# Kernel tuning notes

Measured on AMD Instinct MI355X. Metric: run time of the kernel, lower is better.

## Reference

```python
import jax, jax.numpy as jnp
import numpy as np

DIM = 128        # channel width
HEAD_DIM = 8     # LiteMLA dim per head
BN_EPS = 1e-5
ATT_EPS = 1e-15


def conv2d(x, w, b=None, groups=1):
    # x: NCHW, w: OIHW; stride 1, SAME padding (matches pad=k//2 in torch)
    y = jax.lax.conv_general_dilated(
        x, w, (1, 1), "SAME",
        dimension_numbers=("NCHW", "OIHW", "NCHW"),
        feature_group_count=groups)
    return y if b is None else y + b[None, :, None, None]


def bn_eval(x, g, b, m, v):
    scale = g * jax.lax.rsqrt(v + BN_EPS)
    return (x - m[None, :, None, None]) * scale[None, :, None, None] + b[None, :, None, None]


def hswish(x):
    return x * jnp.clip(x + 3.0, 0.0, 6.0) * (1.0 / 6.0)


def relu_linear_att(qkv):
    # qkv: [B, G*3*d, H, W] with d = HEAD_DIM
    B, C, H, W = qkv.shape
    d = HEAD_DIM
    qkv = qkv.reshape(B, -1, 3 * d, H * W)          # [B, G, 3d, N]
    q = jax.nn.relu(qkv[:, :, :d])                  # [B, G, d, N]
    k = jax.nn.relu(qkv[:, :, d:2 * d])             # [B, G, d, N]
    v = qkv[:, :, 2 * d:]                           # [B, G, d, N]
    v = jnp.concatenate([v, jnp.ones_like(v[:, :, :1])], axis=2)  # pad ones row -> [B, G, d+1, N]
    kv = jnp.einsum("bgdn,bgen->bgde", v, k)        # [B, G, d+1, d]
    out = jnp.einsum("bgde,bgen->bgdn", kv, q)      # [B, G, d+1, N]
    out = out[:, :, :d] / (out[:, :, d:d + 1] + ATT_EPS)
    return out.reshape(B, -1, H, W)                 # [B, G*d, H, W]


def setup_inputs() -> dict:
    key = jax.random.key(0)
    ks = jax.random.split(key, 24)
    dim = DIM
    mid = 6 * dim
    B, H, W = 4, 128, 128

    def w(k, shape, s=0.05):
        return jax.random.normal(k, shape, jnp.float32) * s

    return {
        "ref_features": jax.random.normal(ks[0], (B, dim, H, W), jnp.float32),
        "other_features": jax.random.normal(ks[1], (B, dim, H, W), jnp.float32),
        # 3x3 QKV projection convs (dim -> total_dim = dim)
        "wq": w(ks[2], (dim, dim, 3, 3)), "bq": w(ks[3], (dim,)),
        "wk": w(ks[4], (dim, dim, 3, 3)), "bk": w(ks[5], (dim,)),
        "wv": w(ks[6], (dim, dim, 3, 3)), "bv": w(ks[7], (dim,)),
        # multi-scale aggreg (scale=5): depthwise 5x5 + grouped 1x1 (groups = 3*heads)
        "agg_dw_w": w(ks[8], (3 * dim, 1, 5, 5)),
        "agg_pw_w": w(ks[9], (3 * dim, HEAD_DIM, 1, 1)),
        # attention output proj: 1x1 (2*dim -> dim), no bias, + BN
        "attn_proj_w": w(ks[10], (dim, 2 * dim, 1, 1)),
        "bn1_g": 1.0 + w(ks[11], (dim,)), "bn1_b": w(ks[12], (dim,)),
        "bn1_m": w(ks[13], (dim,), 0.1),
        "bn1_v": jax.random.uniform(ks[14], (dim,), jnp.float32, 0.5, 1.5),
        # MBConv: expand 1x1 (bias, hswish), depthwise 3x3 (bias, hswish), project 1x1 (no bias) + BN
        "mb1_w": w(ks[15], (mid, dim, 1, 1)), "mb1_b": w(ks[16], (mid,)),
        "mb2_w": w(ks[17], (mid, 1, 3, 3)), "mb2_b": w(ks[18], (mid,)),
        "mb3_w": w(ks[19], (dim, mid, 1, 1)),
        "bn2_g": 1.0 + w(ks[20], (dim,)), "bn2_b": w(ks[21], (dim,)),
        "bn2_m": w(ks[22], (dim,), 0.1),
        "bn2_v": jax.random.uniform(ks[23], (dim,), jnp.float32, 0.5, 1.5),
    }


def reference(ref_features, other_features, wq, bq, wk, bk, wv, bv,
              agg_dw_w, agg_pw_w, attn_proj_w, bn1_g, bn1_b, bn1_m, bn1_v,
              mb1_w, mb1_b, mb2_w, mb2_b, mb3_w, bn2_g, bn2_b, bn2_m, bn2_v):
    dim = DIM
    heads = dim // HEAD_DIM
    # QKV via 3x3 convs and concat
    q = conv2d(ref_features, wq, bq)
    k = conv2d(other_features, wk, bk)
    v = conv2d(other_features, wv, bv)
    qkv = jnp.concatenate([q, k, v], axis=1)               # [B, 3*dim, H, W]
    # multi-scale branch (scale 5)
    ms = conv2d(qkv, agg_dw_w, groups=3 * dim)             # depthwise 5x5
    ms = conv2d(ms, agg_pw_w, groups=3 * heads)            # grouped 1x1
    multi = jnp.concatenate([qkv, ms], axis=1)             # [B, 6*dim, H, W]
    # ReLU linear attention + proj(1x1) + BN
    att = relu_linear_att(multi)                           # [B, 2*dim, H, W]
    att = bn_eval(conv2d(att, attn_proj_w), bn1_g, bn1_b, bn1_m, bn1_v)
    attended = ref_features + att
    # local module: residual MBConv
    h = hswish(conv2d(attended, mb1_w, mb1_b))
    h = hswish(conv2d(h, mb2_w, mb2_b, groups=6 * dim))
    h = bn_eval(conv2d(h, mb3_w), bn2_g, bn2_b, bn2_m, bn2_v)
    return attended + h
```

## Files before the change

### kernel.cpp

```cpp
#include <hip/hip_runtime.h>
#include <hip/hip_bf16.h>

#define HH 128
#define WW 128
#define NPIX 16384

using bf16 = __hip_bfloat16;
typedef __attribute__((ext_vector_type(8))) short short8;
typedef __attribute__((ext_vector_type(4))) float f32x4;

__device__ __forceinline__ float b2f(bf16 x){ return __bfloat162float(x); }
__device__ __forceinline__ bf16 f2b(float x){ return __float2bfloat16(x); }
__device__ __forceinline__ unsigned short f2bu(float x){
  bf16 h = __float2bfloat16(x);
  return __builtin_bit_cast(unsigned short, h);
}
__device__ __forceinline__ unsigned short bbits(bf16 x){
  return __builtin_bit_cast(unsigned short, x);
}
__device__ __forceinline__ float u16f(unsigned short u){
  return __bfloat162float(__builtin_bit_cast(bf16, u));
}
__device__ __forceinline__ unsigned int relu2(unsigned int x){
  unsigned int s = x & 0x80008000u;
  unsigned int t = s >> 15;
  unsigned int m = (t << 16) - t;
  return x & ~m;
}
__device__ __forceinline__ float hswish(float x){
  float t = fminf(fmaxf(x + 3.0f, 0.0f), 6.0f);
  return x * t * (1.0f/6.0f);
}

__global__ __launch_bounds__(256) void k_wprep(
    const float* __restrict__ wq, const float* __restrict__ wk,
    const float* __restrict__ wv, const float* __restrict__ bq,
    const float* __restrict__ bk, const float* __restrict__ bv,
    const float* __restrict__ w1, const float* __restrict__ w3,
    bf16* __restrict__ wbf2, float* __restrict__ biasc,
    bf16* __restrict__ w1b, bf16* __restrict__ w3b)
{
  const int idx = blockIdx.x*256 + (int)threadIdx.x;
  if (idx < 384)
    biasc[idx] = (idx < 128) ? bq[idx] : (idx < 256 ? bk[idx-128] : bv[idx-256]);
  if (idx < 98304) {
    w1b[idx] = f2b(w1[idx]);
    w3b[idx] = f2b(w3[idx]);
  }
  if (idx < 384*1152) {
    const int c = idx / 1152, rem = idx % 1152;
    const int tap = rem >> 7, ci = rem & 127;
    const float* wsrc = (c < 128) ? wq : (c < 256 ? wk : wv);
    const int cl = (c < 128) ? c : (c < 256 ? c-128 : c-256);
    wbf2[idx] = f2b(wsrc[(size_t)cl*1152 + ci*9 + tap]);
  }
}

__global__ __launch_bounds__(256) void k_nhwc(
    const float* __restrict__ refB, const float* __restrict__ othB,
    bf16* __restrict__ nh)
{
  const int pt = blockIdx.x & 127;
  const int sidx = blockIdx.x >> 7;
  const float* src = sidx ? othB : refB;
  __shared__ unsigned short t[128][130];
  const int tid = threadIdx.x;
  const int px4 = (tid & 31) * 4;
  const int cq = tid >> 5;
  #pragma unroll
  for (int cb = 0; cb < 16; ++cb) {
    const int c = cb*8 + cq;
    const float4 f = *(const float4*)(src + (size_t)c*NPIX + pt*128 + px4);
    t[px4+0][c] = f2bu(f.x); t[px4+1][c] = f2bu(f.y);
    t[px4+2][c] = f2bu(f.z); t[px4+3][c] = f2bu(f.w);
// ... 62 lines not shown

  #pragma unroll
  for (int cb = 0; cb < 4; ++cb) {
    __syncthreads();
    #pragma unroll
    for (int row = 0; row < 3; ++row) {
      *(uint4*)&lds[row*RSTR + ldsw]     = cur[row][0];
      *(uint4*)&lds[row*RSTR + ldsw + 8] = cur[row][1];
    }
    __syncthreads();
    if (cb < 3) {
      #pragma unroll
      for (int row = 0; row < 3; ++row) {
        const int yy = y + row - 1;
        if (yy >= 0 && yy < HH) {
          const bf16* p = src + (size_t)(yy*WW + sx)*128 + (cb+1)*32 + sp*16;
          nxt[row][0] = *(const uint4*)(p);
          nxt[row][1] = *(const uint4*)(p + 8);
        } else { nxt[row][0] = z4; nxt[row][1] = z4; }
      }
    }
    #pragma unroll
    for (int tap = 0; tap < 9; ++tap) {
      const int trow = tap/3, kx = tap%3;
      const short8 af = *(const short8*)(wbf2
          + (size_t)(cw + l15)*1152 + tap*128 + cb*32 + qd*8);
      const int bbase = trow*RSTR + (l15 + kx)*CSTR + qd*8;
      #pragma unroll
      for (int g = 0; g < 8; ++g) {
        const short8 bfr = *(const short8*)&lds[bbase + g*16*CSTR];
        acc[g] = __builtin_amdgcn_mfma_f32_16x16x32_bf16(af, bfr, acc[g], 0, 0, 0);
      }
    }
    #pragma unroll
    for (int row = 0; row < 3; ++row) {
      cur[row][0] = nxt[row][0];
      cur[row][1] = nxt[row][1];
    }
  }
  #pragma unroll
  for (int r = 0; r < 4; ++r) {
    const int c = cw + qd*4 + r;
    const int gg = c / 24, rr = c % 24;
    bf16* outp = (rr < 8) ? (qbuf + (size_t)(gg*8 + rr)*NPIX)
                          : (kvbuf + (size_t)(gg*16 + (rr-8))*NPIX);
    const float bias = biasc[c];
    #pragma unroll
    for (int g = 0; g < 8; ++g)
      outp[y*WW + g*16 + l15] = f2b(acc[g][r] + bias);
  }
}

#define KVSTR 520
#define ATT_SMEM_BYTES 37120
__global__ __launch_bounds__(256) void k_att_ms(
    const bf16* __restrict__ kvbuf, const bf16* __restrict__ qbuf,
    const float* __restrict__ adw, const float* __restrict__ apw,
    float* __restrict__ part, bf16* __restrict__ msq)
{
  __shared__ __align__(16) unsigned char smem[ATT_SMEM_BYTES];
  const int br = blockIdx.x % 3;
  const int sub = blockIdx.x / 3;
  const int tid = threadIdx.x;
  const int lane = tid & 63;
  const int w = tid >> 6;
  const int qd = lane >> 4, l15 = lane & 15;

  if (br == 0) {
    const int s = sub & 31;
    const int gl = sub >> 5;
    const bf16* bp = kvbuf + (size_t)gl*16*NPIX;
    float (*redm)[9][8] = (float(*)[9][8])smem;
    const int k0 = s*512 + w*128 + qd*8;
    const bf16* ap = bp + (size_t)(8 + (l15 & 7))*NPIX + k0;
    const bf16* bk = bp + (size_t)(l15 & 7)*NPIX + k0;
    const short8 ones8 = {0x3F80,0x3F80,0x3F80,0x3F80,0x3F80,0x3F80,0x3F80,0x3F80};
    f32x4 mac = (f32x4){0.f,0.f,0.f,0.f};
    #pragma unroll
    for (int m = 0; m < 4; ++m) {
      short8 av = *(const short8*)(ap + m*32);
      if (l15 == 8) av = ones8;
      uint4 bu = *(const uint4*)(bk + m*32);
      bu.x = relu2(bu.x); bu.y = relu2(bu.y);
      bu.z = relu2(bu.z); bu.w = relu2(bu.w);
      const short8 bv = __builtin_bit_cast(short8, bu);
      mac = __builtin_amdgcn_mfma_f32_16x16x32_bf16(av, bv, mac, 0, 0, 0);
    }
    #pragma unroll
    for (int r = 0; r < 4; ++r) {
      const int row = qd*4 + r;
      if (l15 < 8 && row < 9) redm[w][row][l15] = mac[r];
    }
    __syncthreads();
    if (tid < 72)
      part[((size_t)gl*32 + s)*72 + tid] =
          redm[0][tid>>3][tid&7] + redm[1][tid>>3][tid&7]
        + redm[2][tid>>3][tid&7] + redm[3][tid>>3][tid&7];

  } else if (br == 1) {
    const int t  = sub & 31;
    const int jj = sub >> 5;
    unsigned short (*sIn)[1056] = (unsigned short(*)[1056])smem;
    float (*dww)[25] = (float(*)[25])(smem + 33792);
    float (*pww)[8]  = (float(*)[8])(smem + 35392);
    float (*redm)[9][8] = (float(*)[9][8])(smem + 35904);
    unsigned short* kvA = (unsigned short*)smem;
    unsigned short* kvB = kvA + 16*KVSTR;

    for (int i = tid; i < 400; i += 256) {
      const int ch = i/25, kk5 = i%25;
      dww[ch][kk5] = adw[(24*jj + 8 + ch)*25 + kk5];
    }
    for (int i = tid; i < 128; i += 256) {
      const int r = i>>3, ii = i&7;
      pww[r][ii] = apw[(24*jj + 8 + r)*8 + ii];
    }
    if (tid < 128) {
      const int ch = tid & 15, r = tid >> 4;
      sIn[ch][r*132 + 0] = 0; sIn[ch][r*132 + 1] = 0;
      sIn[ch][r*132 + 130] = 0; sIn[ch][r*132 + 131] = 0;
    }
    const int y0 = t*4 - 2;
    #pragma unroll
    for (int rep = 0; rep < 8; ++rep) {
      const int L = rep*256 + tid;
      const int col8 = L & 15;
      const int rowc = L >> 4;
      const int r = rowc >> 4, ch = rowc & 15;
      const int gy = y0 + r;
      uint4 pk = make_uint4(0u,0u,0u,0u);
      if (gy >= 0 && gy < HH)
        pk = *(const uint4*)(kvbuf + (size_t)(jj*16 + ch)*NPIX + gy*WW + col8*8);
      unsigned short* dst = &sIn[ch][r*132 + 2 + col8*8];
      *(unsigned int*)(dst + 0) = pk.x;
      *(unsigned int*)(dst + 2) = pk.y;
      *(unsigned int*)(dst + 4) = pk.z;
      *(unsigned int*)(dst + 6) = pk.w;
    }
    __syncthreads();

    const int x = tid & 127;
    const int h = tid >> 7;
    const int rbase = h*2;

    float ko[8][2];
    #pragma unroll
    for (int e=0;e<8;++e){ ko[e][0]=0.f; ko[e][1]=0.f; }
    #pragma unroll
    for (int c=0;c<8;++c) {
      float o0=0.f, o1=0.f;
      #pragma unroll
      for (int rr=0; rr<6; ++rr) {
        const unsigned short* rp = &sIn[c][(rbase+rr)*132 + x];
        #pragma unroll
        for (int dx=0; dx<5; ++dx) {
          const float v = u16f(rp[dx]);
          if (rr <= 4) o0 += dww[c][rr*5+dx]*v;
          if (rr >= 1) o1 += dww[c][(rr-1)*5+dx]*v;
        }
      }
      #pragma unroll
      for (int e=0;e<8;++e){ ko[e][0] += pww[e][c]*o0; ko[e][1] += pww[e][c]*o1; }
    }
    #pragma unroll
    for (int e=0;e<8;++e){ ko[e][0]=fmaxf(ko[e][0],0.f); ko[e][1]=fmaxf(ko[e][1],0.f); }

    float dv[8][2];
    #pragma unroll
    for (int c=0;c<8;++c) {
      float o0=0.f, o1=0.f;
      #pragma unroll
      for (int rr=0; rr<6; ++rr) {
        const unsigned short* rp = &sIn[8+c][(rbase+rr)*132 + x];
        #pragma unroll
        for (int dx=0; dx<5; ++dx) {
          const float v = u16f(rp[dx]);
          if (rr <= 4) o0 += dww[8+c][rr*5+dx]*v;
          if (rr >= 1) o1 += dww[8+c][(rr-1)*5+dx]*v;
        }
      }
      dv[c][0]=o0; dv[c][1]=o1;
    }
    float mv[8][2];
    #pragma unroll
    for (int d=0;d<8;++d) {
      float v0=0.f, v1=0.f;
      #pragma unroll
      for (int i=0;i<8;++i){ v0 += pww[8+d][i]*dv[i][0]; v1 += pww[8+d][i]*dv[i][1]; }
      mv[d][0]=v0; mv[d][1]=v1;
    }

    __syncthreads();
    #pragma unroll
    for (int rr=0; rr<2; ++rr) {
      const int px = (h*2+rr)*128 + x;
      #pragma unroll
      for (int e=0;e<8;++e) kvB[e*KVSTR + px] = f2bu(ko[e][rr]);
      #pragma unroll
      for (int d=0;d<8;++d) kvA[d*KVSTR + px] = f2bu(mv[d][rr]);
      kvA[8*KVSTR + px] = 0x3F80;
    }
    __syncthreads();

    f32x4 mac = (f32x4){0.f,0.f,0.f,0.f};
    #pragma unroll
    for (int m = 0; m < 4; ++m) {
      const int kk = w*128 + m*32 + qd*8;
      const short8 av = *(const short8*)&kvA[l15*KVSTR + kk];
      const short8 bv = *(const short8*)&kvB[l15*KVSTR + kk];
      mac = __builtin_amdgcn_mfma_f32_16x16x32_bf16(av, bv, mac, 0, 0, 0);
    }
    #pragma unroll
    for (int r = 0; r < 4; ++r) {
      const int row = qd*4 + r;
      if (l15 < 8 && row < 9) redm[w][row][l15] = mac[r];
    }
    __syncthreads();
    if (tid < 72)
      part[((size_t)(16+jj)*32 + t)*72 + tid] =
          redm[0][tid>>3][tid&7] + redm[1][tid>>3][tid&7]
        + redm[2][tid>>3][tid&7] + redm[3][tid>>3][tid&7];

  } else {
    const int t  = sub & 31;
    const int jj = sub >> 5;
    unsigned short (*sIn)[1056] = (unsigned short(*)[1056])smem;
    float (*dww)[25] = (float(*)[25])(smem + 16896);
    float (*pww)[8]  = (float(*)[8])(smem + 17696);

    for (int i = tid; i < 200; i += 256)
      dww[i/25][i%25] = adw[(24*jj + i/25)*25 + (i%25)];
    if (tid < 64)
      pww[tid>>3][tid&7] = apw[(24*jj + (tid>>3))*8 + (tid&7)];
    if (tid < 64) {
      const int ch = tid & 7, r = tid >> 3;
      sIn[ch][r*132 + 0] = 0; sIn[ch][r*132 + 1] = 0;
      sIn[ch][r*132 + 130] = 0; sIn[ch][r*132 + 131] = 0;
    }
    const int y0 = t*4 - 2;
    #pragma unroll
    for (int rep = 0; rep < 4; ++rep) {
      const int L = rep*256 + tid;
      const int col8 = L & 15;
      const int rowc = L >> 4;
      const int r = rowc >> 3, ch = rowc & 7;
      const int gy = y0 + r;
      uint4 pk = make_uint4(0u,0u,0u,0u);
      if (gy >= 0 && gy < HH)
        pk = *(const uint4*)(qbuf + (size_t)(jj*8 + ch)*NPIX + gy*WW + col8*8);
      unsigned short* dst = &sIn[ch][r*132 + 2 + col8*8];
      *(unsigned int*)(dst + 0) = pk.x;
      *(unsigned int*)(dst + 2) = pk.y;
      *(unsigned int*)(dst + 4) = pk.z;
      *(unsigned int*)(dst + 6) = pk.w;
    }
    __syncthreads();

    const int x = tid & 127;
    const int h = tid >> 7;
    const int rbase = h*2;
    const int row0 = t*4 + h*2;

    float dq[8][2];
    #pragma unroll
    for (int c=0;c<8;++c) {
      float o0=0.f, o1=0.f;
      #pragma unroll
      for (int rr=0; rr<6; ++rr) {
        const unsigned short* rp = &sIn[c][(rbase+rr)*132 + x];
        #pragma unroll
        for (int dx=0; dx<5; ++dx) {
          const float v = u16f(rp[dx]);
          if (rr <= 4) o0 += dww[c][rr*5+dx]*v;
          if (rr >= 1) o1 += dww[c][(rr-1)*5+dx]*v;
        }
      }
      dq[c][0]=o0; dq[c][1]=o1;
    }
    #pragma unroll
    for (int e=0;e<8;++e) {
      float o0=0.f, o1=0.f;
      #pragma unroll
      for (int i=0;i<8;++i){ o0 += pww[e][i]*dq[i][0]; o1 += pww[e][i]*dq[i][1]; }
      bf16* op = msq + (size_t)(jj*8 + e)*NPIX + row0*WW + x;
      op[0]  = f2b(o0);
      op[WW] = f2b(o1);
    }
  }
}

__global__ __launch_bounds__(256) void k_fold2(
    const float* __restrict__ pjw, const float* __restrict__ part,
    const float* __restrict__ g1, const float* __restrict__ bb1,
    const float* __restrict__ m1, const float* __restrict__ v1,
    bf16* __restrict__ wtb, float* __restrict__ bias2, float* __restrict__ kvf)
{
  const int co = blockIdx.x;
  const int ge = (int)threadIdx.x;
  const int g = ge >> 3, e = ge & 7;
  float kv[8];
  #pragma unroll
  for (int d=0;d<8;++d) kv[d] = 0.f;
  for (int s = 0; s < 32; ++s) {
    const float* pp = part + ((size_t)g*32 + s)*72;
    #pragma unroll
    for (int d=0;d<8;++d) kv[d] += pp[d*8 + e];
  }
  const float sc = g1[co] * rsqrtf(v1[co] + 1e-5f);
  float acc = 0.f;
  #pragma unroll
  for (int d = 0; d < 8; ++d)
    acc += pjw[co*256 + g*8 + d] * kv[d];
  wtb[(size_t)co*256 + ge] = f2b(sc * acc);
  if (ge == 0) bias2[co] = bb1[co] - m1[co]*sc;
  if (co < 32 && ge < 8) {
    float s8 = 0.f;
    for (int s = 0; s < 32; ++s) s8 += part[((size_t)co*32 + s)*72 + 64 + ge];
    kvf[(size_t)co*72 + 64 + ge] = s8;
  }
}

__global__ __launch_bounds__(256) void k_proj_m(
    const bf16* __restrict__ qbuf, const bf16* __restrict__ msq,
    const float* __restrict__ kvf, const bf16* __restrict__ wtb,
    const float* __restrict__ bias2, const float* __restrict__ refB,
    float* __restrict__ attd)
{
  const int n0 = blockIdx.x * 64;
  __shared__ unsigned short lds[64*CSTR];
  __shared__ float kvden[32][8];
  __shared__ float b2s[128];
  const int tid = threadIdx.x;
  kvden[tid>>3][tid&7] = kvf[(size_t)(tid>>3)*72 + 64 + (tid&7)];
  if (tid < 128) b2s[tid] = bias2[tid];
  const int lane = tid & 63;
  const int w = tid >> 6;
  const int qd = lane >> 4, l15 = lane & 15;
  const int px = tid & 63;

// ... 41 lines not shown
      for (int gg = 0; gg < 4; ++gg) {
        const int pxg = n0 + gg*16 + l15;
        attd[(size_t)co*NPIX + pxg] = refB[(size_t)co*NPIX + pxg] + acc[t][gg][r] + bi;
      }
    }
  }
}

__global__ __launch_bounds__(256) void k_mb1_m(
    const float* __restrict__ attd, const bf16* __restrict__ w1b,
    const float* __restrict__ bias, bf16* __restrict__ h1s, int s)
{
  const int pxt = blockIdx.x & 127;
  const int cot = blockIdx.x >> 7;
  const int n0 = pxt*128;
  __shared__ unsigned short lds[128*CSTR];
  const int tid = threadIdx.x;
  const int lane = tid & 63;
  const int wv4 = tid >> 6;
  const int co16 = s*192 + cot*64 + wv4*16;
  const int qd = lane >> 4, l15 = lane & 15;
  f32x4 acc[8];
  #pragma unroll
  for (int g=0; g<8; ++g) acc[g] = (f32x4){0.f,0.f,0.f,0.f};
  const int sx = tid & 127, sp = tid >> 7;
  for (int cb = 0; cb < 4; ++cb) {
    __syncthreads();
    const float* rp = attd + (size_t)(cb*32)*NPIX + n0 + sx;
    for (int cp = sp; cp < 16; cp += 2) {
      const float a0 = rp[(size_t)(2*cp)*NPIX];
      const float a1 = rp[(size_t)(2*cp+1)*NPIX];
      *(unsigned int*)&lds[sx*CSTR + 2*cp] =
          ((unsigned int)f2bu(a1) << 16) | f2bu(a0);
    }
    __syncthreads();
    const short8 af = *(const short8*)(w1b + (size_t)(co16 + l15)*128 + cb*32 + qd*8);
    #pragma unroll
    for (int g = 0; g < 8; ++g) {
      const short8 bfr = *(const short8*)&lds[(g*16 + l15)*CSTR + qd*8];
      acc[g] = __builtin_amdgcn_mfma_f32_16x16x32_bf16(af, bfr, acc[g], 0, 0, 0);
    }
  }
  #pragma unroll
  for (int r = 0; r < 4; ++r) {
    const int co = co16 + qd*4 + r;
    const float bi = bias[co];
    bf16* op = h1s + (size_t)(co - s*192)*NPIX + n0;
    #pragma unroll
    for (int g = 0; g < 8; ++g)
      op[g*16 + l15] = f2b(hswish(acc[g][r] + bi));
  }
}

__global__ __launch_bounds__(256) void k_mb2(
    const bf16* __restrict__ h1s, const float* __restrict__ w,
    const float* __restrict__ bias, bf16* __restrict__ h2s, int s)
{
  const int rt = blockIdx.x & 3;
  const int cl = blockIdx.x >> 2;
  const int cg = s*192 + cl;
  __shared__ unsigned short tile[34][132];
  __shared__ float wc9[9];
  __shared__ float bsh[1];
  const int tid = threadIdx.x;
  if (tid < 9) wc9[tid] = w[cg*9 + tid];
  if (tid == 9) bsh[0] = bias[cg];
  if (tid < 136) {
    const int r = tid >> 2;
    const int csel = tid & 3;
    const int c = (csel == 0) ? 0 : (csel == 1) ? 1 : (csel == 2) ? 130 : 131;
    tile[r][c] = 0;
  }
  const int y0 = rt*32;
  const bf16* in = h1s + (size_t)cl*NPIX;
  for (int i = tid; i < 544; i += 256) {
    const int rr = i >> 4, c8 = i & 15;
    const int gy = y0 - 1 + rr;
    uint4 pk = make_uint4(0u,0u,0u,0u);
    if (gy >= 0 && gy < HH) pk = *(const uint4*)(in + gy*WW + c8*8);
    unsigned short* dst = &tile[rr][2 + c8*8];
    *(unsigned int*)(dst+0)=pk.x; *(unsigned int*)(dst+2)=pk.y;
    *(unsigned int*)(dst+4)=pk.z; *(unsigned int*)(dst+6)=pk.w;
  }
  __syncthreads();
  const int x = tid & 127;
  const int rb = (tid >> 7) * 16;
  float a0,b0,c0,a1,b1,c1,a2,b2,c2;
  {
    const unsigned short* p = &tile[rb][x+1];
    a0=u16f(p[0]); b0=u16f(p[1]); c0=u16f(p[2]);
    p = &tile[rb+1][x+1];
    a1=u16f(p[0]); b1=u16f(p[1]); c1=u16f(p[2]);
  }
  bf16* op = h2s + (size_t)cl*NPIX + (y0+rb)*WW + x;
  #pragma unroll
  for (int j = 0; j < 16; ++j) {
    const unsigned short* p = &tile[rb+j+2][x+1];
    a2=u16f(p[0]); b2=u16f(p[1]); c2=u16f(p[2]);
    float acc = bsh[0] + wc9[0]*a0 + wc9[1]*b0 + wc9[2]*c0
                       + wc9[3]*a1 + wc9[4]*b1 + wc9[5]*c1
                       + wc9[6]*a2 + wc9[7]*b2 + wc9[8]*c2;
    op[j*WW] = f2b(hswish(acc));
    a0=a1; b0=b1; c0=c1; a1=a2; b1=b2; c1=c2;
  }
}

__global__ __launch_bounds__(256) void k_mb31(
    const bf16* __restrict__ h2s, const bf16* __restrict__ w3b,
    float* __restrict__ accb, int s3,
    const float* __restrict__ attd, const bf16* __restrict__ w1b,
    const float* __restrict__ bias1, bf16* __restrict__ h1s, int s1)
{
  __shared__ unsigned short lds[128*CSTR];
  const int tid = threadIdx.x;
  const int lane = tid & 63;
  const int wv4 = tid >> 6;
  const int qd = lane >> 4, l15 = lane & 15;
  const int sx = tid & 127, sp = tid >> 7;

  if (blockIdx.x < 256) {
    const int pxt = blockIdx.x & 127;
    const int cot = blockIdx.x >> 7;
    const int n0 = pxt*128;
    const int co16 = cot*64 + wv4*16;
    f32x4 acc[8];
    #pragma unroll
    for (int g=0; g<8; ++g) acc[g] = (f32x4){0.f,0.f,0.f,0.f};
    for (int cb = 0; cb < 6; ++cb) {
      __syncthreads();
      const bf16* rp = h2s + (size_t)(cb*32)*NPIX + n0 + sx;
      for (int cp = sp; cp < 16; cp += 2) {
        const unsigned short a0 = bbits(rp[(size_t)(2*cp)*NPIX]);
        const unsigned short a1 = bbits(rp[(size_t)(2*cp+1)*NPIX]);
        *(unsigned int*)&lds[sx*CSTR + 2*cp] = ((unsigned int)a1 << 16) | a0;
      }
      __syncthreads();
      const short8 af = *(const short8*)(w3b + (size_t)(co16 + l15)*768 + s3*192 + cb*32 + qd*8);
      #pragma unroll
      for (int g = 0; g < 8; ++g) {
        const short8 bfr = *(const short8*)&lds[(g*16 + l15)*CSTR + qd*8];
        acc[g] = __builtin_amdgcn_mfma_f32_16x16x32_bf16(af, bfr, acc[g], 0, 0, 0);
      }
    }
    #pragma unroll
    for (int r = 0; r < 4; ++r) {
      const int co = co16 + qd*4 + r;
      float* op = accb + (size_t)co*NPIX + n0;
      if (s3 == 0) {
        #pragma unroll
        for (int g = 0; g < 8; ++g) op[g*16 + l15] = acc[g][r];
      } else {
        #pragma unroll
        for (int g = 0; g < 8; ++g) op[g*16 + l15] += acc[g][r];
      }
    }
  } else {
    const int bid = blockIdx.x - 256;
    const int pxt = bid & 127;
    const int cot = bid >> 7;
    const int n0 = pxt*128;
    const int co16 = s1*192 + cot*64 + wv4*16;
    f32x4 acc[8];
    #pragma unroll
    for (int g=0; g<8; ++g) acc[g] = (f32x4){0.f,0.f,0.f,0.f};
    for (int cb = 0; cb < 4; ++cb) {
      __syncthreads();
      const float* rp = attd + (size_t)(cb*32)*NPIX + n0 + sx;
      for (int cp = sp; cp < 16; cp += 2) {
        const float a0 = rp[(size_t)(2*cp)*NPIX];
        const float a1 = rp[(size_t)(2*cp+1)*NPIX];
        *(unsigned int*)&lds[sx*CSTR + 2*cp] =
            ((unsigned int)f2bu(a1) << 16) | f2bu(a0);
      }
      __syncthreads();
      const short8 af = *(const short8*)(w1b + (size_t)(co16 + l15)*128 + cb*32 + qd*8);
      #pragma unroll
      for (int g = 0; g < 8; ++g) {
        const short8 bfr = *(const short8*)&lds[(g*16 + l15)*CSTR + qd*8];
        acc[g] = __builtin_amdgcn_mfma_f32_16x16x32_bf16(af, bfr, acc[g], 0, 0, 0);
      }
    }
    #pragma unroll
    for (int r = 0; r < 4; ++r) {
      const int co = co16 + qd*4 + r;
      const float bi = bias1[co];
      bf16* op = h1s + (size_t)(co - s1*192)*NPIX + n0;
      #pragma unroll
      for (int g = 0; g < 8; ++g)
        op[g*16 + l15] = f2b(hswish(acc[g][r] + bi));
    }
  }
}

__global__ __launch_bounds__(256) void k_mb3f(
    const bf16* __restrict__ h2s, const bf16* __restrict__ w3b,
    const float* __restrict__ accb,
    const float* __restrict__ g2, const float* __restrict__ b2p,
    const float* __restrict__ m2, const float* __restrict__ v2,
    float* __restrict__ attd)
{
  const int pxt = blockIdx.x & 127;
  const int cot = blockIdx.x >> 7;
  const int n0 = pxt*128;
  __shared__ unsigned short lds[128*CSTR];
  const int tid = threadIdx.x;
  const int lane = tid & 63;
  const int wv4 = tid >> 6;
  const int co16 = cot*64 + wv4*16;
  const int qd = lane >> 4, l15 = lane & 15;
  f32x4 acc[8];
  #pragma unroll
  for (int g=0; g<8; ++g) acc[g] = (f32x4){0.f,0.f,0.f,0.f};
  const int sx = tid & 127, sp = tid >> 7;
  for (int cb = 0; cb < 6; ++cb) {
    __syncthreads();
    const bf16* rp = h2s + (size_t)(cb*32)*NPIX + n0 + sx;
    for (int cp = sp; cp < 16; cp += 2) {
      const unsigned short a0 = bbits(rp[(size_t)(2*cp)*NPIX]);
      const unsigned short a1 = bbits(rp[(size_t)(2*cp+1)*NPIX]);
      *(unsigned int*)&lds[sx*CSTR + 2*cp] = ((unsigned int)a1 << 16) | a0;
    }
    __syncthreads();
    const short8 af = *(const short8*)(w3b + (size_t)(co16 + l15)*768 + 576 + cb*32 + qd*8);
    #pragma unroll
    for (int g = 0; g < 8; ++g) {
      const short8 bfr = *(const short8*)&lds[(g*16 + l15)*CSTR + qd*8];
      acc[g] = __builtin_amdgcn_mfma_f32_16x16x32_bf16(af, bfr, acc[g], 0, 0, 0);
    }
  }
  #pragma unroll
  for (int r = 0; r < 4; ++r) {
    const int co = co16 + qd*4 + r;
    const float scale = g2[co] * rsqrtf(v2[co] + 1e-5f);
    const float bb = b2p[co];
    const float mm = m2[co];
    #pragma unroll
    for (int g = 0; g < 8; ++g) {
      const size_t idx = (size_t)co*NPIX + n0 + g*16 + l15;
      const float val = accb[idx] + acc[g][r];
      const float y = (val - mm)*scale + bb;
      attd[idx] = attd[idx] + y;
    }
  }
}

extern "C" void kernel_launch(void* const* d_in, const int* in_sizes, int n_in,
                              void* d_out, int out_size, void* d_ws, size_t ws_size,
                              hipStream_t stream)
{
  const float* ref = (const float*)d_in[0];
  const float* oth = (const float*)d_in[1];
  const float* wq  = (const float*)d_in[2];
  const float* bq  = (const float*)d_in[3];
  const float* wk  = (const float*)d_in[4];
  const float* bk  = (const float*)d_in[5];
  const float* wv  = (const float*)d_in[6];
  const float* bv  = (const float*)d_in[7];
  const float* adw = (const float*)d_in[8];
  const float* apw = (const float*)d_in[9];
  const float* pjw = (const float*)d_in[10];
  const float* g1  = (const float*)d_in[11];
  const float* b1  = (const float*)d_in[12];
  const float* m1  = (const float*)d_in[13];
  const float* v1  = (const float*)d_in[14];
  const float* w1  = (const float*)d_in[15];
  const float* bb1 = (const float*)d_in[16];
  const float* w2  = (const float*)d_in[17];
  const float* bb2 = (const float*)d_in[18];
  const float* w3  = (const float*)d_in[19];
  const float* g2  = (const float*)d_in[20];
  const float* b2p = (const float*)d_in[21];
  const float* m2  = (const float*)d_in[22];
  const float* v2  = (const float*)d_in[23];

  char* ws = (char*)d_ws;
  bf16*  wbf2  = (bf16*)(ws + 0);
  float* biasc = (float*)(ws + 884736);
  bf16*  w1b   = (bf16*)(ws + 886272);
  bf16*  w3b   = (bf16*)(ws + 1082880);
  bf16*  kvbuf = (bf16*)(ws + 1279488);
  bf16*  qbuf  = (bf16*)(ws + 9668096);
  bf16*  nh    = (bf16*)(ws + 13862400);
  bf16*  msq   = (bf16*)(ws + 13862400);
  float* part  = (float*)(ws + 22251008);
  float* kvf   = (float*)(ws + 22545920);
  bf16*  wtb   = (bf16*)(ws + 22555136);
  float* bias2 = (float*)(ws + 22620672);
  float* accb  = (float*)(ws + 1279488);
  bf16*  h1s   = (bf16*)(ws + 9668096);
  bf16*  h2s   = (bf16*)(ws + 15959552);

  k_wprep<<<1728, 256, 0, stream>>>(wq, wk, wv, bq, bk, bv, w1, w3, wbf2, biasc, w1b, w3b);

  for (int b = 0; b < 4; ++b) {
    const float* refB = ref + (size_t)b*128*NPIX;
    const float* othB = oth + (size_t)b*128*NPIX;
    float* attd = (float*)d_out + (size_t)b*128*NPIX;

    k_nhwc   <<<256,  256, 0, stream>>>(refB, othB, nh);
    k_conv   <<<768,  256, 0, stream>>>(nh, wbf2, biasc, kvbuf, qbuf);
    k_att_ms <<<1536, 256, 0, stream>>>(kvbuf, qbuf, adw, apw, part, msq);
    k_fold2  <<<128,  256, 0, stream>>>(pjw, part, g1, b1, m1, v1, wtb, bias2, kvf);
    k_proj_m <<<256,  256, 0, stream>>>(qbuf, msq, kvf, wtb, bias2, refB, attd);

    k_mb1_m  <<<384,  256, 0, stream>>>(attd, w1b, bb1, h1s, 0);
    k_mb2    <<<768,  256, 0, stream>>>(h1s, w2, bb2, h2s, 0);
    for (int s = 0; s < 3; ++s) {
      k_mb31 <<<640,  256, 0, stream>>>(h2s, w3b, accb, s, attd, w1b, bb1, h1s, s+1);
      k_mb2  <<<768,  256, 0, stream>>>(h1s, w2, bb2, h2s, s+1);
    }
    k_mb3f   <<<256,  256, 0, stream>>>(h2s, w3b, accb, g2, b2p, m2, v2, attd);
  }
}
```

Before: 919.5 us.

## Fuse depthwise 3x3 MBConv stage into the pointwise projection GEMM kernels

The standalone depthwise 3x3 kernel (k_mb2) is removed. Its computation now runs inside the 1x1 projection kernels: each block loads three halo rows of 32 channels, computes depthwise plus hswish into LDS, then feeds the result to MFMA. The h1 buffer is ping-ponged between two workspace slots, which removes the h2 round trip through global memory and four launches per batch. In exchange, blocks are now organised per image row with heavier LDS use (about 36 KB), and each block recomputes the depthwise conv for its own output-channel tile, so that work is duplicated across the two cot tiles.

```diff
diff --git a/kernel.cpp b/kernel.cpp
--- a/kernel.cpp
+++ b/kernel.cpp
@@ -568,96 +568,112 @@
   }
 }
 
-__global__ __launch_bounds__(256) void k_mb2(
-    const bf16* __restrict__ h1s, const float* __restrict__ w,
-    const float* __restrict__ bias, bf16* __restrict__ h2s, int s)
-{
-  const int rt = blockIdx.x & 3;
-  const int cl = blockIdx.x >> 2;
-  const int cg = s*192 + cl;
-  __shared__ unsigned short tile[34][132];
-  __shared__ float wc9[9];
-  __shared__ float bsh[1];
-  const int tid = threadIdx.x;
-  if (tid < 9) wc9[tid] = w[cg*9 + tid];
-  if (tid == 9) bsh[0] = bias[cg];
-  if (tid < 136) {
-    const int r = tid >> 2;
-    const int csel = tid & 3;
-    const int c = (csel == 0) ? 0 : (csel == 1) ? 1 : (csel == 2) ? 130 : 131;
-    tile[r][c] = 0;
-  }
-  const int y0 = rt*32;
-  const bf16* in = h1s + (size_t)cl*NPIX;
-  for (int i = tid; i < 544; i += 256) {
-    const int rr = i >> 4, c8 = i & 15;
-    const int gy = y0 - 1 + rr;
-    uint4 pk = make_uint4(0u,0u,0u,0u);
-    if (gy >= 0 && gy < HH) pk = *(const uint4*)(in + gy*WW + c8*8);
-    unsigned short* dst = &tile[rr][2 + c8*8];
-    *(unsigned int*)(dst+0)=pk.x; *(unsigned int*)(dst+2)=pk.y;
-    *(unsigned int*)(dst+4)=pk.z; *(unsigned int*)(dst+6)=pk.w;
-  }
-  __syncthreads();
-  const int x = tid & 127;
-  const int rb = (tid >> 7) * 16;
-  float a0,b0,c0,a1,b1,c1,a2,b2,c2;
-  {
-    const unsigned short* p = &tile[rb][x+1];
-    a0=u16f(p[0]); b0=u16f(p[1]); c0=u16f(p[2]);
-    p = &tile[rb+1][x+1];
-    a1=u16f(p[0]); b1=u16f(p[1]); c1=u16f(p[2]);
-  }
-  bf16* op = h2s + (size_t)cl*NPIX + (y0+rb)*WW + x;
-  #pragma unroll
-  for (int j = 0; j < 16; ++j) {
-    const unsigned short* p = &tile[rb+j+2][x+1];
-    a2=u16f(p[0]); b2=u16f(p[1]); c2=u16f(p[2]);
-    float acc = bsh[0] + wc9[0]*a0 + wc9[1]*b0 + wc9[2]*c0
-                       + wc9[3]*a1 + wc9[4]*b1 + wc9[5]*c1
-                       + wc9[6]*a2 + wc9[7]*b2 + wc9[8]*c2;
-    op[j*WW] = f2b(hswish(acc));
-    a0=a1; b0=b1; c0=c1; a1=a2; b1=b2; c1=c2;
-  }
-}
-
-__global__ __launch_bounds__(256) void k_mb31(
-    const bf16* __restrict__ h2s, const bf16* __restrict__ w3b,
+__device__ __forceinline__ void mb23_acc(
+    const bf16* __restrict__ h1, const bf16* __restrict__ w3b,
+    const float* __restrict__ w2, const float* __restrict__ bb2,
+    int s3, int y, int cot, unsigned char* smem, int tid, f32x4 acc[8])
+{
+  unsigned short* tileH = (unsigned short*)smem;
+  unsigned short* ldsB  = (unsigned short*)(smem + 25344);
+  float* dwws = (float*)(smem + 35584);
+  float* bsh2 = (float*)(smem + 36736);
+  const int lane = tid & 63;
+  const int wv4 = tid >> 6;
+  const int qd = lane >> 4, l15 = lane & 15;
+  const int co16 = cot*64 + wv4*16;
+
+  if (tid < 96) {
+    const int ch = tid & 31, r = tid >> 5;
+    *(unsigned int*)&tileH[ch*396 + r*132 + 0] = 0u;
+    *(unsigned int*)&tileH[ch*396 + r*132 + 130] = 0u;
+  }
+
+  for (int cb = 0; cb < 6; ++cb) {
+    for (int i = tid; i < 288; i += 256) {
+      const int ch = i/9, k9 = i%9;
+      dwws[ch*9+k9] = w2[((size_t)(s3*192 + cb*32 + ch))*9 + k9];
+    }
+    if (tid < 32) bsh2[tid] = bb2[s3*192 + cb*32 + tid];
+    for (int u = tid; u < 1536; u += 256) {
+      const int c8 = u & 15;
+      const int t2 = u >> 4;
+      const int ch = t2 & 31, r = t2 >> 5;
+      const int gy = y + r - 1;
+      uint4 pk = make_uint4(0u,0u,0u,0u);
+      if (gy >= 0 && gy < HH)
+        pk = *(const uint4*)(h1 + (size_t)(cb*32+ch)*NPIX + gy*WW + c8*8);
+      unsigned short* dst = &tileH[ch*396 + r*132 + 2 + c8*8];
+      *(unsigned int*)(dst+0)=pk.x; *(unsigned int*)(dst+2)=pk.y;
+      *(unsigned int*)(dst+4)=pk.z; *(unsigned int*)(dst+6)=pk.w;
+    }
+    __syncthreads();
+    const int px0 = (tid & 15) * 8;
+    const int chp = (tid >> 4) * 2;
+    float outp[2][8];
+    #pragma unroll
+    for (int cc = 0; cc < 2; ++cc) {
+      const int ch = chp + cc;
+      float v[3][12];
+      #pragma unroll
+      for (int r = 0; r < 3; ++r) {
+        const unsigned int* rp = (const unsigned int*)&tileH[ch*396 + r*132 + px0];
+        #pragma unroll
+        for (int k = 0; k < 6; ++k) {
+          const unsigned int u = rp[k];
+          v[r][2*k]   = u16f((unsigned short)(u & 0xffffu));
+          v[r][2*k+1] = u16f((unsigned short)(u >> 16));
+        }
+      }
+      const float* wc = &dwws[ch*9];
+      const float bi = bsh2[ch];
+      #pragma unroll
+      for (int j = 0; j < 8; ++j) {
+        float a = bi;
+        #pragma unroll
+        for (int r = 0; r < 3; ++r)
+          #pragma unroll
+          for (int dx = 0; dx < 3; ++dx)
+            a += wc[r*3+dx] * v[r][j+dx+1];
+        outp[cc][j] = hswish(a);
+      }
+    }
+    #pragma unroll
+    for (int j = 0; j < 8; ++j) {
+      const unsigned int pk2 = ((unsigned int)f2bu(outp[1][j]) << 16) | f2bu(outp[0][j]);
+      *(unsigned int*)&ldsB[(px0+j)*40 + chp] = pk2;
+    }
+    __syncthreads();
+    const short8 af = *(const short8*)(w3b + (size_t)(co16 + l15)*768 + s3*192 + cb*32 + qd*8);
+    #pragma unroll
+    for (int g = 0; g < 8; ++g) {
+      const short8 bfr = *(const short8*)&ldsB[(g*16 + l15)*40 + qd*8];
+      acc[g] = __builtin_amdgcn_mfma_f32_16x16x32_bf16(af, bfr, acc[g], 0, 0, 0);
+    }
+  }
+}
+
+__global__ __launch_bounds__(256) void k_mb31f(
+    const bf16* __restrict__ h1rd, const bf16* __restrict__ w3b,
+    const float* __restrict__ w2, const float* __restrict__ bb2,
     float* __restrict__ accb, int s3,
     const float* __restrict__ attd, const bf16* __restrict__ w1b,
-    const float* __restrict__ bias1, bf16* __restrict__ h1s, int s1)
-{
-  __shared__ unsigned short lds[128*CSTR];
+    const float* __restrict__ bias1, bf16* __restrict__ h1wr, int s1)
+{
+  __shared__ __align__(16) unsigned char smem[36864];
   const int tid = threadIdx.x;
   const int lane = tid & 63;
   const int wv4 = tid >> 6;
   const int qd = lane >> 4, l15 = lane & 15;
-  const int sx = tid & 127, sp = tid >> 7;
 
   if (blockIdx.x < 256) {
-    const int pxt = blockIdx.x & 127;
+    const int y = blockIdx.x & 127;
     const int cot = blockIdx.x >> 7;
-    const int n0 = pxt*128;
+    f32x4 acc[8];
+    #pragma unroll
+    for (int g=0; g<8; ++g) acc[g] = (f32x4){0.f,0.f,0.f,0.f};
+    mb23_acc(h1rd, w3b, w2, bb2, s3, y, cot, smem, tid, acc);
+    const int n0 = y*128;
     const int co16 = cot*64 + wv4*16;
-    f32x4 acc[8];
-    #pragma unroll
-    for (int g=0; g<8; ++g) acc[g] = (f32x4){0.f,0.f,0.f,0.f};
-    for (int cb = 0; cb < 6; ++cb) {
-      __syncthreads();
-      const bf16* rp = h2s + (size_t)(cb*32)*NPIX + n0 + sx;
-      for (int cp = sp; cp < 16; cp += 2) {
-        const unsigned short a0 = bbits(rp[(size_t)(2*cp)*NPIX]);
-        const unsigned short a1 = bbits(rp[(size_t)(2*cp+1)*NPIX]);
-        *(unsigned int*)&lds[sx*CSTR + 2*cp] = ((unsigned int)a1 << 16) | a0;
-      }
-      __syncthreads();
-      const short8 af = *(const short8*)(w3b + (size_t)(co16 + l15)*768 + s3*192 + cb*32 + qd*8);
-      #pragma unroll
-      for (int g = 0; g < 8; ++g) {
-        const short8 bfr = *(const short8*)&lds[(g*16 + l15)*CSTR + qd*8];
-        acc[g] = __builtin_amdgcn_mfma_f32_16x16x32_bf16(af, bfr, acc[g], 0, 0, 0);
-      }
-    }
     #pragma unroll
     for (int r = 0; r < 4; ++r) {
       const int co = co16 + qd*4 + r;
@@ -671,6 +687,7 @@
       }
     }
   } else {
+    unsigned short* lds = (unsigned short*)smem;
     const int bid = blockIdx.x - 256;
     const int pxt = bid & 127;
     const int cot = bid >> 7;
@@ -679,6 +696,7 @@
     f32x4 acc[8];
     #pragma unroll
     for (int g=0; g<8; ++g) acc[g] = (f32x4){0.f,0.f,0.f,0.f};
+    const int sx = tid & 127, sp = tid >> 7;
     for (int cb = 0; cb < 4; ++cb) {
       __syncthreads();
       const float* rp = attd + (size_t)(cb*32)*NPIX + n0 + sx;
@@ -700,7 +718,7 @@
     for (int r = 0; r < 4; ++r) {
       const int co = co16 + qd*4 + r;
       const float bi = bias1[co];
-      bf16* op = h1s + (size_t)(co - s1*192)*NPIX + n0;
+      bf16* op = h1wr + (size_t)(co - s1*192)*NPIX + n0;
       #pragma unroll
       for (int g = 0; g < 8; ++g)
         op[g*16 + l15] = f2b(hswish(acc[g][r] + bi));
@@ -708,42 +726,27 @@
   }
 }
 
-__global__ __launch_bounds__(256) void k_mb3f(
-    const bf16* __restrict__ h2s, const bf16* __restrict__ w3b,
+__global__ __launch_bounds__(256) void k_mb3ff(
+    const bf16* __restrict__ h1rd, const bf16* __restrict__ w3b,
+    const float* __restrict__ w2, const float* __restrict__ bb2,
     const float* __restrict__ accb,
     const float* __restrict__ g2, const float* __restrict__ b2p,
     const float* __restrict__ m2, const float* __restrict__ v2,
     float* __restrict__ attd)
 {
-  const int pxt = blockIdx.x & 127;
-  const int cot = blockIdx.x >> 7;
-  const int n0 = pxt*128;
-  __shared__ unsigned short lds[128*CSTR];
+  __shared__ __align__(16) unsigned char smem[36864];
   const int tid = threadIdx.x;
   const int lane = tid & 63;
   const int wv4 = tid >> 6;
+  const int qd = lane >> 4, l15 = lane & 15;
+  const int y = blockIdx.x & 127;
+  const int cot = blockIdx.x >> 7;
+  f32x4 acc[8];
+  #pragma unroll
+  for (int g=0; g<8; ++g) acc[g] = (f32x4){0.f,0.f,0.f,0.f};
+  mb23_acc(h1rd, w3b, w2, bb2, 3, y, cot, smem, tid, acc);
+  const int n0 = y*128;
   const int co16 = cot*64 + wv4*16;
-  const int qd = lane >> 4, l15 = lane & 15;
-  f32x4 acc[8];
-  #pragma unroll
-  for (int g=0; g<8; ++g) acc[g] = (f32x4){0.f,0.f,0.f,0.f};
-  const int sx = tid & 127, sp = tid >> 7;
-  for (int cb = 0; cb < 6; ++cb) {
-    __syncthreads();
-    const bf16* rp = h2s + (size_t)(cb*32)*NPIX + n0 + sx;
-    for (int cp = sp; cp < 16; cp += 2) {
-      const unsigned short a0 = bbits(rp[(size_t)(2*cp)*NPIX]);
-      const unsigned short a1 = bbits(rp[(size_t)(2*cp+1)*NPIX]);
-      *(unsigned int*)&lds[sx*CSTR + 2*cp] = ((unsigned int)a1 << 16) | a0;
-    }
-    __syncthreads();
-    const short8 af = *(const short8*)(w3b + (size_t)(co16 + l15)*768 + 576 + cb*32 + qd*8);
-    #pragma unroll
-    for (int g = 0; g < 8; ++g) {
-      const short8 bfr = *(const short8*)&lds[(g*16 + l15)*CSTR + qd*8];
-      acc[g] = __builtin_amdgcn_mfma_f32_16x16x32_bf16(af, bfr, acc[g], 0, 0, 0);
-    }
-  }
   #pragma unroll
   for (int r = 0; r < 4; ++r) {
     const int co = co16 + qd*4 + r;
@@ -754,8 +757,8 @@
     for (int g = 0; g < 8; ++g) {
       const size_t idx = (size_t)co*NPIX + n0 + g*16 + l15;
       const float val = accb[idx] + acc[g][r];
-      const float y = (val - mm)*scale + bb;
-      attd[idx] = attd[idx] + y;
+      const float yv = (val - mm)*scale + bb;
+      attd[idx] = attd[idx] + yv;
     }
   }
 }
@@ -803,8 +806,8 @@
   bf16*  wtb   = (bf16*)(ws + 22555136);
   float* bias2 = (float*)(ws + 22620672);
   float* accb  = (float*)(ws + 1279488);
-  bf16*  h1s   = (bf16*)(ws + 9668096);
-  bf16*  h2s   = (bf16*)(ws + 15959552);
+  bf16*  h1a   = (bf16*)(ws + 9668096);
+  bf16*  h1b   = (bf16*)(ws + 15959552);
 
   k_wprep<<<1728, 256, 0, stream>>>(wq, wk, wv, bq, bk, bv, w1, w3, wbf2, biasc, w1b, w3b);
 
@@ -819,12 +822,14 @@
     k_fold2  <<<128,  256, 0, stream>>>(pjw, part, g1, b1, m1, v1, wtb, bias2, kvf);
     k_proj_m <<<256,  256, 0, stream>>>(qbuf, msq, kvf, wtb, bias2, refB, attd);
 
-    k_mb1_m  <<<384,  256, 0, stream>>>(attd, w1b, bb1, h1s, 0);
-    k_mb2    <<<768,  256, 0, stream>>>(h1s, w2, bb2, h2s, 0);
+    k_mb1_m  <<<384,  256, 0, stream>>>(attd, w1b, bb1, h1a, 0);
     for (int s = 0; s < 3; ++s) {
-      k_mb31 <<<640,  256, 0, stream>>>(h2s, w3b, accb, s, attd, w1b, bb1, h1s, s+1);
-      k_mb2  <<<768,  256, 0, stream>>>(h1s, w2, bb2, h2s, s+1);
-    }
-    k_mb3f   <<<256,  256, 0, stream>>>(h2s, w3b, accb, g2, b2p, m2, v2, attd);
-  }
-}
+      bf16* h1rd = (s & 1) ? h1b : h1a;
+      bf16* h1wr = (s & 1) ? h1a : h1b;
+      k_mb31f<<<640, 256, 0, stream>>>(h1rd, w3b, w2, bb2, accb, s,
+                                       attd, w1b, bb1, h1wr, s+1);
+    }
+    k_mb3ff  <<<256,  256, 0, stream>>>(h1b, w3b, w2, bb2, accb,
+                                        g2, b2p, m2, v2, attd);
+  }
+}
```

Result: slower. 1.041 ms (+13.3%).

## Remap depthwise conv to horizontal pixel pairs and halve att_ms shared memory

Applied to the files above, without the earlier changes.

The depthwise 5x5 in the multiscale attention kernel now has each thread compute two horizontally adjacent pixels from packed 32-bit LDS reads, instead of two vertically adjacent pixels from 16-bit reads. The k/v branch stages its 8 k channels, computes, then reuses the same buffer for the 8 v channels, which roughly halves shared memory per block. Outputs and kv staging stores are packed into 32-bit writes, and MFMA row indices are clamped to the smaller kvA buffer. The aim is fewer LDS instructions and higher occupancy, at the cost of an extra reload phase and barrier in the kv branch.

```diff
diff --git a/kernel.cpp b/kernel.cpp
--- a/kernel.cpp
+++ b/kernel.cpp
@@ -20,6 +20,10 @@
 }
 __device__ __forceinline__ float u16f(unsigned short u){
   return __bfloat162float(__builtin_bit_cast(bf16, u));
+}
+__device__ __forceinline__ void bf2x(unsigned int u, float& a, float& b){
+  a = u16f((unsigned short)(u & 0xffffu));
+  b = u16f((unsigned short)(u >> 16));
 }
 __device__ __forceinline__ unsigned int relu2(unsigned int x){
   unsigned int s = x & 0x80008000u;
@@ -188,7 +192,7 @@
 }
 
 #define KVSTR 520
-#define ATT_SMEM_BYTES 37120
+#define ATT_SMEM_BYTES 20160
 __global__ __launch_bounds__(256) void k_att_ms(
     const bf16* __restrict__ kvbuf, const bf16* __restrict__ qbuf,
     const float* __restrict__ adw, const float* __restrict__ apw,
@@ -237,11 +241,11 @@
     const int t  = sub & 31;
     const int jj = sub >> 5;
     unsigned short (*sIn)[1056] = (unsigned short(*)[1056])smem;
-    float (*dww)[25] = (float(*)[25])(smem + 33792);
-    float (*pww)[8]  = (float(*)[8])(smem + 35392);
-    float (*redm)[9][8] = (float(*)[9][8])(smem + 35904);
+    float (*dww)[25] = (float(*)[25])(smem + 16896);
+    float (*pww)[8]  = (float(*)[8])(smem + 18496);
+    float (*redm)[9][8] = (float(*)[9][8])(smem + 19008);
     unsigned short* kvA = (unsigned short*)smem;
-    unsigned short* kvB = kvA + 16*KVSTR;
+    unsigned short* kvB = kvA + 9*KVSTR;
 
     for (int i = tid; i < 400; i += 256) {
       const int ch = i/25, kk5 = i%25;
@@ -251,18 +255,22 @@
       const int r = i>>3, ii = i&7;
       pww[r][ii] = apw[(24*jj + 8 + r)*8 + ii];
     }
-    if (tid < 128) {
-      const int ch = tid & 15, r = tid >> 4;
-      sIn[ch][r*132 + 0] = 0; sIn[ch][r*132 + 1] = 0;
-      sIn[ch][r*132 + 130] = 0; sIn[ch][r*132 + 131] = 0;
+    if (tid < 64) {
+      const int ch = tid & 7, r = tid >> 3;
+      *(unsigned int*)&sIn[ch][r*132 + 0] = 0u;
+      *(unsigned int*)&sIn[ch][r*132 + 130] = 0u;
     }
     const int y0 = t*4 - 2;
-    #pragma unroll
-    for (int rep = 0; rep < 8; ++rep) {
+    const int xp = (tid & 63)*2;
+    const int row = tid >> 6;
+    float ko[8][2], mv[8][2];
+
+    #pragma unroll
+    for (int rep = 0; rep < 4; ++rep) {
       const int L = rep*256 + tid;
       const int col8 = L & 15;
       const int rowc = L >> 4;
-      const int r = rowc >> 4, ch = rowc & 15;
+      const int r = rowc >> 3, ch = rowc & 7;
       const int gy = y0 + r;
       uint4 pk = make_uint4(0u,0u,0u,0u);
       if (gy >= 0 && gy < HH)
@@ -274,82 +282,96 @@
       *(unsigned int*)(dst + 6) = pk.w;
     }
     __syncthreads();
-
-    const int x = tid & 127;
-    const int h = tid >> 7;
-    const int rbase = h*2;
-
-    float ko[8][2];
     #pragma unroll
     for (int e=0;e<8;++e){ ko[e][0]=0.f; ko[e][1]=0.f; }
     #pragma unroll
     for (int c=0;c<8;++c) {
       float o0=0.f, o1=0.f;
       #pragma unroll
-      for (int rr=0; rr<6; ++rr) {
-        const unsigned short* rp = &sIn[c][(rbase+rr)*132 + x];
+      for (int rr=0; rr<5; ++rr) {
+        const unsigned int* rp = (const unsigned int*)&sIn[c][(row+rr)*132 + xp];
+        float v0,v1,v2,v3,v4,v5;
+        bf2x(rp[0], v0, v1); bf2x(rp[1], v2, v3); bf2x(rp[2], v4, v5);
+        const float* wr = &dww[c][rr*5];
+        o0 += wr[0]*v0; o0 += wr[1]*v1; o0 += wr[2]*v2; o0 += wr[3]*v3; o0 += wr[4]*v4;
+        o1 += wr[0]*v1; o1 += wr[1]*v2; o1 += wr[2]*v3; o1 += wr[3]*v4; o1 += wr[4]*v5;
+      }
+      #pragma unroll
+      for (int e=0;e<8;++e){ ko[e][0] += pww[e][c]*o0; ko[e][1] += pww[e][c]*o1; }
+    }
+    #pragma unroll
+    for (int e=0;e<8;++e){ ko[e][0]=fmaxf(ko[e][0],0.f); ko[e][1]=fmaxf(ko[e][1],0.f); }
+    __syncthreads();
+
+    #pragma unroll
+    for (int rep = 0; rep < 4; ++rep) {
+      const int L = rep*256 + tid;
+      const int col8 = L & 15;
+      const int rowc = L >> 4;
+      const int r = rowc >> 3, ch = rowc & 7;
+      const int gy = y0 + r;
+      uint4 pk = make_uint4(0u,0u,0u,0u);
+      if (gy >= 0 && gy < HH)
+        pk = *(const uint4*)(kvbuf + (size_t)(jj*16 + 8 + ch)*NPIX + gy*WW + col8*8);
+      unsigned short* dst = &sIn[ch][r*132 + 2 + col8*8];
+      *(unsigned int*)(dst + 0) = pk.x;
+      *(unsigned int*)(dst + 2) = pk.y;
+      *(unsigned int*)(dst + 4) = pk.z;
+      *(unsigned int*)(dst + 6) = pk.w;
+    }
+    __syncthreads();
+    {
+      float dv[8][2];
+      #pragma unroll
+      for (int c=0;c<8;++c) {
+        float o0=0.f, o1=0.f;
         #pragma unroll
-        for (int dx=0; dx<5; ++dx) {
-          const float v = u16f(rp[dx]);
-          if (rr <= 4) o0 += dww[c][rr*5+dx]*v;
-          if (rr >= 1) o1 += dww[c][(rr-1)*5+dx]*v;
+        for (int rr=0; rr<5; ++rr) {
+          const unsigned int* rp = (const unsigned int*)&sIn[c][(row+rr)*132 + xp];
+          float v0,v1,v2,v3,v4,v5;
+          bf2x(rp[0], v0, v1); bf2x(rp[1], v2, v3); bf2x(rp[2], v4, v5);
+          const float* wr = &dww[8+c][rr*5];
+          o0 += wr[0]*v0; o0 += wr[1]*v1; o0 += wr[2]*v2; o0 += wr[3]*v3; o0 += wr[4]*v4;
+          o1 += wr[0]*v1; o1 += wr[1]*v2; o1 += wr[2]*v3; o1 += wr[3]*v4; o1 += wr[4]*v5;
         }
-      }
-      #pragma unroll
-      for (int e=0;e<8;++e){ ko[e][0] += pww[e][c]*o0; ko[e][1] += pww[e][c]*o1; }
-    }
-    #pragma unroll
-    for (int e=0;e<8;++e){ ko[e][0]=fmaxf(ko[e][0],0.f); ko[e][1]=fmaxf(ko[e][1],0.f); }
-
-    float dv[8][2];
-    #pragma unroll
-    for (int c=0;c<8;++c) {
-      float o0=0.f, o1=0.f;
-      #pragma unroll
-      for (int rr=0; rr<6; ++rr) {
-        const unsigned short* rp = &sIn[8+c][(rbase+rr)*132 + x];
+        dv[c][0]=o0; dv[c][1]=o1;
+      }
+      #pragma unroll
+      for (int d=0;d<8;++d) {
+        float v0=0.f, v1=0.f;
         #pragma unroll
-        for (int dx=0; dx<5; ++dx) {
-          const float v = u16f(rp[dx]);
-          if (rr <= 4) o0 += dww[8+c][rr*5+dx]*v;
-          if (rr >= 1) o1 += dww[8+c][(rr-1)*5+dx]*v;
-        }
-      }
-      dv[c][0]=o0; dv[c][1]=o1;
-    }
-    float mv[8][2];
-    #pragma unroll
-    for (int d=0;d<8;++d) {
-      float v0=0.f, v1=0.f;
-      #pragma unroll
-      for (int i=0;i<8;++i){ v0 += pww[8+d][i]*dv[i][0]; v1 += pww[8+d][i]*dv[i][1]; }
-      mv[d][0]=v0; mv[d][1]=v1;
-    }
-
-    __syncthreads();
-    #pragma unroll
-    for (int rr=0; rr<2; ++rr) {
-      const int px = (h*2+rr)*128 + x;
-      #pragma unroll
-      for (int e=0;e<8;++e) kvB[e*KVSTR + px] = f2bu(ko[e][rr]);
-      #pragma unroll
-      for (int d=0;d<8;++d) kvA[d*KVSTR + px] = f2bu(mv[d][rr]);
-      kvA[8*KVSTR + px] = 0x3F80;
-    }
-    __syncthreads();
-
+        for (int i=0;i<8;++i){ v0 += pww[8+d][i]*dv[i][0]; v1 += pww[8+d][i]*dv[i][1]; }
+        mv[d][0]=v0; mv[d][1]=v1;
+      }
+    }
+    __syncthreads();
+
+    const int px = row*128 + xp;
+    #pragma unroll
+    for (int e=0;e<8;++e)
+      *(unsigned int*)&kvB[e*KVSTR + px] =
+          ((unsigned int)f2bu(ko[e][1]) << 16) | f2bu(ko[e][0]);
+    #pragma unroll
+    for (int d=0;d<8;++d)
+      *(unsigned int*)&kvA[d*KVSTR + px] =
+          ((unsigned int)f2bu(mv[d][1]) << 16) | f2bu(mv[d][0]);
+    *(unsigned int*)&kvA[8*KVSTR + px] = 0x3F803F80u;
+    __syncthreads();
+
+    const int ra = (l15 < 9) ? l15 : 0;
+    const int rb = l15 & 7;
     f32x4 mac = (f32x4){0.f,0.f,0.f,0.f};
     #pragma unroll
     for (int m = 0; m < 4; ++m) {
       const int kk = w*128 + m*32 + qd*8;
-      const short8 av = *(const short8*)&kvA[l15*KVSTR + kk];
-      const short8 bv = *(const short8*)&kvB[l15*KVSTR + kk];
+      const short8 av = *(const short8*)&kvA[ra*KVSTR + kk];
+      const short8 bv = *(const short8*)&kvB[rb*KVSTR + kk];
       mac = __builtin_amdgcn_mfma_f32_16x16x32_bf16(av, bv, mac, 0, 0, 0);
     }
     #pragma unroll
     for (int r = 0; r < 4; ++r) {
-      const int row = qd*4 + r;
-      if (l15 < 8 && row < 9) redm[w][row][l15] = mac[r];
+      const int rw = qd*4 + r;
+      if (l15 < 8 && rw < 9) redm[w][rw][l15] = mac[r];
     }
     __syncthreads();
     if (tid < 72)
@@ -370,8 +392,8 @@
       pww[tid>>3][tid&7] = apw[(24*jj + (tid>>3))*8 + (tid&7)];
     if (tid < 64) {
       const int ch = tid & 7, r = tid >> 3;
-      sIn[ch][r*132 + 0] = 0; sIn[ch][r*132 + 1] = 0;
-      sIn[ch][r*132 + 130] = 0; sIn[ch][r*132 + 131] = 0;
+      *(unsigned int*)&sIn[ch][r*132 + 0] = 0u;
+      *(unsigned int*)&sIn[ch][r*132 + 130] = 0u;
     }
     const int y0 = t*4 - 2;
     #pragma unroll
@@ -392,24 +414,22 @@
     }
     __syncthreads();
 
-    const int x = tid & 127;
-    const int h = tid >> 7;
-    const int rbase = h*2;
-    const int row0 = t*4 + h*2;
+    const int xp = (tid & 63)*2;
+    const int row = tid >> 6;
+    const int row0 = t*4 + row;
 
     float dq[8][2];
     #pragma unroll
     for (int c=0;c<8;++c) {
       float o0=0.f, o1=0.f;
       #pragma unroll
-      for (int rr=0; rr<6; ++rr) {
-        const unsigned short* rp = &sIn[c][(rbase+rr)*132 + x];
-        #pragma unroll
-        for (int dx=0; dx<5; ++dx) {
-          const float v = u16f(rp[dx]);
-          if (rr <= 4) o0 += dww[c][rr*5+dx]*v;
-          if (rr >= 1) o1 += dww[c][(rr-1)*5+dx]*v;
-        }
+      for (int rr=0; rr<5; ++rr) {
+        const unsigned int* rp = (const unsigned int*)&sIn[c][(row+rr)*132 + xp];
+        float v0,v1,v2,v3,v4,v5;
+        bf2x(rp[0], v0, v1); bf2x(rp[1], v2, v3); bf2x(rp[2], v4, v5);
+        const float* wr = &dww[c][rr*5];
+        o0 += wr[0]*v0; o0 += wr[1]*v1; o0 += wr[2]*v2; o0 += wr[3]*v3; o0 += wr[4]*v4;
+        o1 += wr[0]*v1; o1 += wr[1]*v2; o1 += wr[2]*v3; o1 += wr[3]*v4; o1 += wr[4]*v5;
       }
       dq[c][0]=o0; dq[c][1]=o1;
     }
@@ -418,9 +438,8 @@
       float o0=0.f, o1=0.f;
       #pragma unroll
       for (int i=0;i<8;++i){ o0 += pww[e][i]*dq[i][0]; o1 += pww[e][i]*dq[i][1]; }
-      bf16* op = msq + (size_t)(jj*8 + e)*NPIX + row0*WW + x;
-      op[0]  = f2b(o0);
-      op[WW] = f2b(o1);
+      *(unsigned int*)(msq + (size_t)(jj*8 + e)*NPIX + row0*WW + xp) =
+          ((unsigned int)f2bu(o1) << 16) | f2bu(o0);
     }
   }
 }
```

Result: faster. 773.5 us (-15.9%).
